# Optimization experiments

Measured on AMD Instinct MI355X. Metric: run time of the kernel, lower is better.

## Reference

```python
import jax, jax.numpy as jnp
import numpy as np

B, S, OBS, NINS, H, NBLK = 1024, 512, 5, 2, 32, 4
EPS = 1e-6


def setup_inputs() -> dict:
    key = jax.random.key(0)
    ks = jax.random.split(key, 10)
    obs_sequence = jax.random.normal(ks[0], (B, S, OBS), jnp.float32)
    prev_actions = jax.random.normal(ks[1], (B, S, NINS), jnp.float32)
    fan_in = OBS + NINS
    # xavier-uniform input projection
    lim_in = np.sqrt(6.0 / (fan_in + H))
    W_in = jax.random.uniform(ks[2], (H, fan_in), jnp.float32, -lim_in, lim_in)
    b_in = jnp.zeros((H,), jnp.float32)
    rms_w = jnp.ones((NBLK, H), jnp.float32)
    # LSTMCell default init: U(-1/sqrt(H), 1/sqrt(H)); gate order i,f,g,o
    s = 1.0 / np.sqrt(H)
    W_ih = jax.random.uniform(ks[3], (NBLK, 4 * H, H), jnp.float32, -s, s)
    W_hh = jax.random.uniform(ks[4], (NBLK, 4 * H, H), jnp.float32, -s, s)
    b_ih = jax.random.uniform(ks[5], (NBLK, 4 * H), jnp.float32, -s, s)
    b_hh = jax.random.uniform(ks[6], (NBLK, 4 * H), jnp.float32, -s, s)
    # heads: kaiming-uniform (linear, fan_in) scaled by 1e-3, zero bias
    lim_h = np.sqrt(3.0 / H)
    head_w = jax.random.uniform(ks[7], (NINS, H), jnp.float32, -lim_h, lim_h) * 1e-3
    head_b = jnp.zeros((NINS,), jnp.float32)
    return dict(obs_sequence=obs_sequence, prev_actions=prev_actions,
                W_in=W_in, b_in=b_in, rms_w=rms_w,
                W_ih=W_ih, W_hh=W_hh, b_ih=b_ih, b_hh=b_hh,
                head_w=head_w, head_b=head_b)


def reference(obs_sequence, prev_actions, W_in, b_in, rms_w,
              W_ih, W_hh, b_ih, b_hh, head_w, head_b):
    batch = obs_sequence.shape[0]
    hdim = W_in.shape[0]
    x = jnp.concatenate([obs_sequence, prev_actions], axis=-1) @ W_in.T + b_in  # [B,S,H]
    xs = jnp.swapaxes(x, 0, 1)  # [S,B,H] for scan over time
    h0 = jnp.zeros((NBLK, batch, hdim), x.dtype)
    c0 = jnp.zeros((NBLK, batch, hdim), x.dtype)

    def step(carry, xt):
        h, c = carry
        hs, cs = [], []
        for k in range(NBLK):  # small fixed stack of distinct blocks
            rms = jnp.sqrt(jnp.mean(xt * xt, axis=-1, keepdims=True) + EPS)
            xn = rms_w[k] * (xt / rms)
            gates = xn @ W_ih[k].T + b_ih[k] + h[k] @ W_hh[k].T + b_hh[k]  # [B,4H]
            i, f, g, o = jnp.split(gates, 4, axis=-1)
            c_new = jax.nn.sigmoid(f) * c[k] + jax.nn.sigmoid(i) * jnp.tanh(g)
            h_new = jax.nn.sigmoid(o) * jnp.tanh(c_new)
            xt = xt + h_new  # residual
            hs.append(h_new)
            cs.append(c_new)
        return (jnp.stack(hs), jnp.stack(cs)), xt

    (hT, cT), ys = jax.lax.scan(step, (h0, c0), xs)  # ys: [S,B,H]
    raw = jnp.einsum('sbh,ih->ibs', ys, head_w) + head_b[:, None, None]  # [NINS,B,S]
    out = jnp.sign(raw) * (jnp.exp(jnp.abs(raw)) - 1.0)  # symexp
    lim = jnp.array([5.0, 10.0], out.dtype)[:, None, None]
    out = jnp.clip(out, -lim, lim)
    return out, hT, cT
```

## Files before the change

### kernel.cpp

```cpp
#include <hip/hip_runtime.h>


constexpr int B_ = 1024, S_ = 512, OBS_ = 5, NINS_ = 2, H_ = 32, NBLK_ = 4;
constexpr int SUP_ = 4;
constexpr int TT_ = S_ / SUP_;
constexpr float EPS_ = 1e-6f;
constexpr float LOG2E_ = 1.4426950408889634f;

typedef __fp16 h2 __attribute__((ext_vector_type(2)));
typedef __fp16 h8 __attribute__((ext_vector_type(8)));
typedef float  f4 __attribute__((ext_vector_type(4)));
typedef int    i4 __attribute__((ext_vector_type(4)));

__device__ __forceinline__ float rcp_(float x) { return __builtin_amdgcn_rcpf(x); }
__device__ __forceinline__ float rsq_(float x) { return __builtin_amdgcn_rsqf(x); }
__device__ __forceinline__ float ex2_(float x) { return __builtin_amdgcn_exp2f(x); }
__device__ __forceinline__ h2 pk_(float a, float b) {
  return __builtin_amdgcn_cvt_pkrtz(a, b);
}
__device__ __forceinline__ h8 pk8_(f4 lo, f4 hi) {
  i4 q;
  q[0] = __builtin_bit_cast(int, pk_(lo[0], lo[1]));
  q[1] = __builtin_bit_cast(int, pk_(lo[2], lo[3]));
  q[2] = __builtin_bit_cast(int, pk_(hi[0], hi[1]));
  q[3] = __builtin_bit_cast(int, pk_(hi[2], hi[3]));
  return __builtin_bit_cast(h8, q);
}
__device__ __forceinline__ f4 mfma_(h8 a, h8 b, f4 c) {
  return __builtin_amdgcn_mfma_f32_16x16x32_f16(a, b, c, 0, 0, 0);
}
__device__ __forceinline__ f4 sg4_(f4 a) {
  f4 r;
  r[0] = rcp_(1.f + ex2_(-a[0]));
  r[1] = rcp_(1.f + ex2_(-a[1]));
  r[2] = rcp_(1.f + ex2_(-a[2]));
  r[3] = rcp_(1.f + ex2_(-a[3]));
  return r;
}
__device__ __forceinline__ f4 th4_(f4 a) {
  f4 r;
  r[0] = fmaf(2.f, rcp_(1.f + ex2_(-a[0])), -1.f);
  r[1] = fmaf(2.f, rcp_(1.f + ex2_(-a[1])), -1.f);
  r[2] = fmaf(2.f, rcp_(1.f + ex2_(-a[2])), -1.f);
  r[3] = fmaf(2.f, rcp_(1.f + ex2_(-a[3])), -1.f);
  return r;
}
__device__ __forceinline__ f4 thc4_(f4 c) {
  constexpr float M = 2.f * LOG2E_;
  f4 r;
  r[0] = fmaf(2.f, rcp_(1.f + ex2_(-M * c[0])), -1.f);
  r[1] = fmaf(2.f, rcp_(1.f + ex2_(-M * c[1])), -1.f);
  r[2] = fmaf(2.f, rcp_(1.f + ex2_(-M * c[2])), -1.f);
  r[3] = fmaf(2.f, rcp_(1.f + ex2_(-M * c[3])), -1.f);
  return r;
}
__device__ __forceinline__ float dot44_(f4 a, f4 x, f4 b2, f4 y) {
  float s = a[0] * x[0];
  s = fmaf(a[1], x[1], s); s = fmaf(a[2], x[2], s); s = fmaf(a[3], x[3], s);
  s = fmaf(b2[0], y[0], s); s = fmaf(b2[1], y[1], s);
  s = fmaf(b2[2], y[2], s); s = fmaf(b2[3], y[3], s);
  return s;
}
__device__ __forceinline__ float psw16_(float v, bool re) {
#if __has_builtin(__builtin_amdgcn_permlane16_swap)
  auto r = __builtin_amdgcn_permlane16_swap(
      __builtin_bit_cast(int, v), __builtin_bit_cast(int, v), false, false);
  return __builtin_bit_cast(float, re ? (int)r[1] : (int)r[0]);
#else
  return __shfl_xor(v, 16);
#endif
}
__device__ __forceinline__ float psw32_(float v, bool lo) {
#if __has_builtin(__builtin_amdgcn_permlane32_swap)
  auto r = __builtin_amdgcn_permlane32_swap(
      __builtin_bit_cast(int, v), __builtin_bit_cast(int, v), false, false);
  return __builtin_bit_cast(float, lo ? (int)r[1] : (int)r[0]);
#else
  return __shfl_xor(v, 32);
#endif
}

#define BLK_STEP(XT0, XT1) do {                                            \
    float _ss = dot44_((XT0), (XT1), (XT1), (XT0));                        \
    _ss = dot44_((XT0), (XT0), (XT1), (XT1));                              \
    _ss += psw16_(_ss, re_);                                               \
    _ss += psw32_(_ss, lo_);                                               \
    const float _rinv = rsq_(_ss * (1.0f / 32.0f) + EPS_);                 \
    const h8 _bh = pk8_(hv0, hv1);                                         \
    f4 _ah0 = mfma_(wh[0], _bh, biasv[0]);                                 \
    f4 _ah1 = mfma_(wh[1], _bh, biasv[1]);                                 \
    f4 _ah2 = mfma_(wh[2], _bh, biasv[2]);                                 \
    f4 _ah3 = mfma_(wh[3], _bh, biasv[3]);                                 \
    f4 _ah4 = mfma_(wh[4], _bh, biasv[4]);                                 \
    f4 _ah5 = mfma_(wh[5], _bh, biasv[5]);                                 \
    f4 _ah6 = mfma_(wh[6], _bh, biasv[6]);                                 \
    f4 _ah7 = mfma_(wh[7], _bh, biasv[7]);                                 \
    const f4 _rs0 = rw0v * _rinv, _rs1 = rw1v * _rinv;                     \
    const h8 _bx = pk8_((XT0) * _rs0, (XT1) * _rs1);                       \
    const f4 _gi0 = mfma_(wx[0], _bx, _ah0);                               \
    const f4 _gi1 = mfma_(wx[1], _bx, _ah1);                               \
    const f4 _gf0 = mfma_(wx[2], _bx, _ah2);                               \
    const f4 _gf1 = mfma_(wx[3], _bx, _ah3);                               \
    const f4 _gg0 = mfma_(wx[4], _bx, _ah4);                               \
    const f4 _gg1 = mfma_(wx[5], _bx, _ah5);                               \
    const f4 _go0 = mfma_(wx[6], _bx, _ah6);                               \
    const f4 _go1 = mfma_(wx[7], _bx, _ah7);                               \
    const f4 _si0 = sg4_(_gi0), _si1 = sg4_(_gi1);                         \
    const f4 _sf0 = sg4_(_gf0), _sf1 = sg4_(_gf1);                         \
    const f4 _tg0 = th4_(_gg0), _tg1 = th4_(_gg1);                         \
    const f4 _so0 = sg4_(_go0), _so1 = sg4_(_go1);                         \
    c0 = _sf0 * c0 + _si0 * _tg0;                                          \
    c1 = _sf1 * c1 + _si1 * _tg1;                                          \
    hv0 = _so0 * thc4_(c0);                                                \
    hv1 = _so1 * thc4_(c1);                                                \
    (XT0) += hv0;                                                          \
    (XT1) += hv1;                                                          \
  } while (0)

__global__ __launch_bounds__(256, 1) void garch_mfma6_kernel(
    const float* __restrict__ obs, const float* __restrict__ prev,
    const float* __restrict__ W_in, const float* __restrict__ b_in,
    const float* __restrict__ rms_w,
    const float* __restrict__ W_ih, const float* __restrict__ W_hh,
    const float* __restrict__ b_ih, const float* __restrict__ b_hh,
    const float* __restrict__ head_w, const float* __restrict__ head_b,
    float* __restrict__ out) {
  const int tid  = threadIdx.x;
  const int k    = tid >> 6;
  const int lane = tid & 63;
  const int g    = lane >> 4;
  const int b    = lane & 15;
  const int bg   = blockIdx.x * 16 + b;
  const bool re_ = ((lane >> 4) & 1) == 0;
  const bool lo_ = (lane < 32);

  __shared__ __align__(16) float xslot[3][2][SUP_][16][36];

  h8 wx[8], wh[8];
  f4 biasv[8];
  {
    const size_t wb = (size_t)k * 128 * 32;
#pragma unroll
    for (int mi = 0; mi < 8; ++mi) {
      const float scl = (mi == 4 || mi == 5) ? 2.f * LOG2E_ : LOG2E_;
      const int row = 16 * mi + b;
      const float* px = W_ih + wb + (size_t)row * 32;
      f4 x0 = *(const f4*)(px + 4 * g);
      f4 x1 = *(const f4*)(px + 16 + 4 * g);
      wx[mi] = pk8_(x0 * scl, x1 * scl);
      const float* ph = W_hh + wb + (size_t)row * 32;
      f4 h0v = *(const f4*)(ph + 4 * g);
      f4 h1v = *(const f4*)(ph + 16 + 4 * g);
      wh[mi] = pk8_(h0v * scl, h1v * scl);
      f4 bv;
#pragma unroll
      for (int r = 0; r < 4; ++r) {
        const int gr = k * 128 + 16 * mi + 4 * g + r;
        bv[r] = (b_ih[gr] + b_hh[gr]) * scl;
      }
      biasv[mi] = bv;
    }
  }
  f4 rw0v, rw1v;
#pragma unroll
  for (int r = 0; r < 4; ++r) {
    rw0v[r] = rms_w[k * 32 + 4 * g + r];
    rw1v[r] = rms_w[k * 32 + 16 + 4 * g + r];
  }

  h8 winA0 = {}, winA1 = {};
  f4 bin0v = {}, bin1v = {};
  const float* obs_b = nullptr; const float* prev_b = nullptr;
  f4 cin[SUP_] = {}, nin[SUP_] = {};
  if (k == 0) {
    f4 lo0, lo1; const f4 z = {};
#pragma unroll
    for (int r = 0; r < 4; ++r) {
      const int kk = 4 * g + r;
      lo0[r] = (kk < 7) ? W_in[(size_t)b * 7 + kk] : 0.f;
      lo1[r] = (kk < 7) ? W_in[(size_t)(16 + b) * 7 + kk] : 0.f;
    }
    winA0 = pk8_(lo0, z);
    winA1 = pk8_(lo1, z);
#pragma unroll
    for (int r = 0; r < 4; ++r) {
      bin0v[r] = b_in[4 * g + r];
      bin1v[r] = b_in[16 + 4 * g + r];
    }
    obs_b  = obs  + (size_t)bg * S_ * OBS_;
    prev_b = prev + (size_t)bg * S_ * NINS_;
#pragma unroll
    for (int s = 0; s < SUP_; ++s) {
      const float* o = obs_b + (size_t)s * OBS_;
      if (g == 0)      { cin[s][0] = o[0]; cin[s][1] = o[1]; cin[s][2] = o[2]; cin[s][3] = o[3]; }
      else if (g == 1) { cin[s][0] = o[4]; cin[s][1] = prev_b[2 * s]; cin[s][2] = prev_b[2 * s + 1]; cin[s][3] = 0.f; }
    }
  }
  f4 hw00 = {}, hw01 = {}, hw10 = {}, hw11 = {};
  float hb0 = 0.f, hb1 = 0.f;
  if (k == 3) {
#pragma unroll
    for (int r = 0; r < 4; ++r) {
      hw00[r] = head_w[4 * g + r]      * LOG2E_;
      hw01[r] = head_w[16 + 4 * g + r] * LOG2E_;
      hw10[r] = head_w[32 + 4 * g + r] * LOG2E_;
      hw11[r] = head_w[48 + 4 * g + r] * LOG2E_;
    }
    hb0 = head_b[0] * LOG2E_;
    hb1 = head_b[1] * LOG2E_;
  }

  f4 c0 = {}, c1 = {}, hv0 = {}, hv1 = {};

  float* out_y  = out;
  float* out_hT = out + (size_t)NINS_ * B_ * S_;
  float* out_cT = out_hT + (size_t)NBLK_ * B_ * H_;

  for (int tau = 0; tau < TT_ + NBLK_ - 1; ++tau) {
    __syncthreads();
    const int tt = tau - k;
    if (tt < 0 || tt >= TT_) continue;
    const int t0 = SUP_ * tt;
    const int wp = tau & 1, rp = (tau + 1) & 1;

    f4 x0[SUP_], x1[SUP_];
    if (k == 0) {
      if (tt + 1 < TT_) {
#pragma unroll
        for (int s = 0; s < SUP_; ++s) {
          const int t = t0 + SUP_ + s;
          const float* o = obs_b + (size_t)t * OBS_;
          if (g == 0)      { nin[s][0] = o[0]; nin[s][1] = o[1]; nin[s][2] = o[2]; nin[s][3] = o[3]; }
          else if (g == 1) { nin[s][0] = o[4]; nin[s][1] = prev_b[2 * t]; nin[s][2] = prev_b[2 * t + 1]; nin[s][3] = 0.f; }
        }
      }
      const f4 z = {};
#pragma unroll
      for (int s = 0; s < SUP_; ++s) {
        const h8 binp = pk8_(cin[s], z);
        x0[s] = mfma_(winA0, binp, bin0v);
        x1[s] = mfma_(winA1, binp, bin1v);
      }
    } else {
#pragma unroll
      for (int s = 0; s < SUP_; ++s) {
        x0[s] = *(const f4*)&xslot[k - 1][rp][s][b][4 * g];
        x1[s] = *(const f4*)&xslot[k - 1][rp][s][b][16 + 4 * g];
      }
    }

#pragma unroll
    for (int s = 0; s < SUP_; ++s) {
      BLK_STEP(x0[s], x1[s]);
    }

    if (k < 3) {
#pragma unroll
      for (int s = 0; s < SUP_; ++s) {
        *(f4*)&xslot[k][wp][s][b][4 * g]      = x0[s];
        *(f4*)&xslot[k][wp][s][b][16 + 4 * g] = x1[s];
      }
    } else {
      float p0[SUP_], p1[SUP_];
#pragma unroll
      for (int s = 0; s < SUP_; ++s) {
        float a = dot44_(hw00, x0[s], hw01, x1[s]);
        float bq = dot44_(hw10, x0[s], hw11, x1[s]);
        a += psw16_(a, re_); a += psw32_(a, lo_);
        bq += psw16_(bq, re_); bq += psw32_(bq, lo_);
        p0[s] = a + hb0;
        p1[s] = bq + hb1;
      }
      if (lane < 16) {
        f4 v0, v1;
#pragma unroll
        for (int s = 0; s < SUP_; ++s) {
          v0[s] = copysignf(fminf(ex2_(fabsf(p0[s])) - 1.f, 5.f),  p0[s]);
          v1[s] = copysignf(fminf(ex2_(fabsf(p1[s])) - 1.f, 10.f), p1[s]);
        }
        *(f4*)&out_y[(size_t)bg * S_ + t0]                   = v0;
        *(f4*)&out_y[(size_t)B_ * S_ + (size_t)bg * S_ + t0] = v1;
      }
    }

    if (tt == TT_ - 1) {
      float* hp = out_hT + ((size_t)k * B_ + bg) * H_;
      float* cp = out_cT + ((size_t)k * B_ + bg) * H_;
#pragma unroll
      for (int r = 0; r < 4; ++r) {
        hp[4 * g + r]      = hv0[r];
        hp[16 + 4 * g + r] = hv1[r];
        cp[4 * g + r]      = c0[r];
        cp[16 + 4 * g + r] = c1[r];
      }
    }

    if (k == 0) {
#pragma unroll
      for (int s = 0; s < SUP_; ++s) cin[s] = nin[s];
    }
  }
}

extern "C" void kernel_launch(void* const* d_in, const int* in_sizes, int n_in,
                              void* d_out, int out_size, void* d_ws, size_t ws_size,
                              hipStream_t stream) {
  (void)in_sizes; (void)n_in; (void)d_ws; (void)ws_size; (void)out_size;
  garch_mfma6_kernel<<<dim3(B_ / 16), dim3(256), 0, stream>>>(
      (const float*)d_in[0],
      (const float*)d_in[1],
      (const float*)d_in[2],
      (const float*)d_in[3],
      (const float*)d_in[4],
      (const float*)d_in[5],
      (const float*)d_in[6],
      (const float*)d_in[7],
      (const float*)d_in[8],
      (const float*)d_in[9],
      (const float*)d_in[10],
      (float*)d_out);
}
```

Before: 465.8 us.

## Hoist input-gate MFMAs off recurrence chain and merge activation reciprocals

Splits each block step so the RMS-norm and input-projection MFMAs for all SUP_ sub-steps are issued together before the recurrent loop, leaving only the hidden-state MFMAs on the serial dependency chain. The gate activations are rewritten to share reciprocals: sigmoid(i)*tanh(g) and sigmoid(o)*tanh(c) are each computed with one rcp over a product of denominators, cutting transcendental ops. This costs more live registers for the precomputed gate tiles (32 f4 values) and risks overflow or inf in the combined denominators for large gate magnitudes.

```diff
diff --git a/kernel.cpp b/kernel.cpp
--- a/kernel.cpp
+++ b/kernel.cpp
@@ -29,29 +29,16 @@
 __device__ __forceinline__ f4 mfma_(h8 a, h8 b, f4 c) {
   return __builtin_amdgcn_mfma_f32_16x16x32_f16(a, b, c, 0, 0, 0);
 }
-__device__ __forceinline__ f4 sg4_(f4 a) {
+__device__ __forceinline__ f4 e4n_(f4 a) {
   f4 r;
-  r[0] = rcp_(1.f + ex2_(-a[0]));
-  r[1] = rcp_(1.f + ex2_(-a[1]));
-  r[2] = rcp_(1.f + ex2_(-a[2]));
-  r[3] = rcp_(1.f + ex2_(-a[3]));
+  r[0] = ex2_(-a[0]); r[1] = ex2_(-a[1]);
+  r[2] = ex2_(-a[2]); r[3] = ex2_(-a[3]);
   return r;
 }
-__device__ __forceinline__ f4 th4_(f4 a) {
+__device__ __forceinline__ f4 rcp4_(f4 a) {
   f4 r;
-  r[0] = fmaf(2.f, rcp_(1.f + ex2_(-a[0])), -1.f);
-  r[1] = fmaf(2.f, rcp_(1.f + ex2_(-a[1])), -1.f);
-  r[2] = fmaf(2.f, rcp_(1.f + ex2_(-a[2])), -1.f);
-  r[3] = fmaf(2.f, rcp_(1.f + ex2_(-a[3])), -1.f);
-  return r;
-}
-__device__ __forceinline__ f4 thc4_(f4 c) {
-  constexpr float M = 2.f * LOG2E_;
-  f4 r;
-  r[0] = fmaf(2.f, rcp_(1.f + ex2_(-M * c[0])), -1.f);
-  r[1] = fmaf(2.f, rcp_(1.f + ex2_(-M * c[1])), -1.f);
-  r[2] = fmaf(2.f, rcp_(1.f + ex2_(-M * c[2])), -1.f);
-  r[3] = fmaf(2.f, rcp_(1.f + ex2_(-M * c[3])), -1.f);
+  r[0] = rcp_(a[0]); r[1] = rcp_(a[1]);
+  r[2] = rcp_(a[2]); r[3] = rcp_(a[3]);
   return r;
 }
 __device__ __forceinline__ float dot44_(f4 a, f4 x, f4 b2, f4 y) {
@@ -80,44 +67,20 @@
 #endif
 }
 
-#define BLK_STEP(XT0, XT1) do {                                            \
-    float _ss = dot44_((XT0), (XT1), (XT1), (XT0));                        \
-    _ss = dot44_((XT0), (XT0), (XT1), (XT1));                              \
-    _ss += psw16_(_ss, re_);                                               \
-    _ss += psw32_(_ss, lo_);                                               \
-    const float _rinv = rsq_(_ss * (1.0f / 32.0f) + EPS_);                 \
-    const h8 _bh = pk8_(hv0, hv1);                                         \
-    f4 _ah0 = mfma_(wh[0], _bh, biasv[0]);                                 \
-    f4 _ah1 = mfma_(wh[1], _bh, biasv[1]);                                 \
-    f4 _ah2 = mfma_(wh[2], _bh, biasv[2]);                                 \
-    f4 _ah3 = mfma_(wh[3], _bh, biasv[3]);                                 \
-    f4 _ah4 = mfma_(wh[4], _bh, biasv[4]);                                 \
-    f4 _ah5 = mfma_(wh[5], _bh, biasv[5]);                                 \
-    f4 _ah6 = mfma_(wh[6], _bh, biasv[6]);                                 \
-    f4 _ah7 = mfma_(wh[7], _bh, biasv[7]);                                 \
-    const f4 _rs0 = rw0v * _rinv, _rs1 = rw1v * _rinv;                     \
-    const h8 _bx = pk8_((XT0) * _rs0, (XT1) * _rs1);                       \
-    const f4 _gi0 = mfma_(wx[0], _bx, _ah0);                               \
-    const f4 _gi1 = mfma_(wx[1], _bx, _ah1);                               \
-    const f4 _gf0 = mfma_(wx[2], _bx, _ah2);                               \
-    const f4 _gf1 = mfma_(wx[3], _bx, _ah3);                               \
-    const f4 _gg0 = mfma_(wx[4], _bx, _ah4);                               \
-    const f4 _gg1 = mfma_(wx[5], _bx, _ah5);                               \
-    const f4 _go0 = mfma_(wx[6], _bx, _ah6);                               \
-    const f4 _go1 = mfma_(wx[7], _bx, _ah7);                               \
-    const f4 _si0 = sg4_(_gi0), _si1 = sg4_(_gi1);                         \
-    const f4 _sf0 = sg4_(_gf0), _sf1 = sg4_(_gf1);                         \
-    const f4 _tg0 = th4_(_gg0), _tg1 = th4_(_gg1);                         \
-    const f4 _so0 = sg4_(_go0), _so1 = sg4_(_go1);                         \
-    c0 = _sf0 * c0 + _si0 * _tg0;                                          \
-    c1 = _sf1 * c1 + _si1 * _tg1;                                          \
-    hv0 = _so0 * thc4_(c0);                                                \
-    hv1 = _so1 * thc4_(c1);                                                \
-    (XT0) += hv0;                                                          \
-    (XT1) += hv1;                                                          \
+#define ACT_TILE(GI, GF, GG, GO, C, HV) do {                               \
+    const f4 _one = {1.f, 1.f, 1.f, 1.f};                                  \
+    const f4 _Ei = e4n_(GI);                                               \
+    const f4 _Eg = e4n_(GG);                                               \
+    const f4 _Ef = e4n_(GF);                                               \
+    const f4 _sitg = (_one - _Eg) * rcp4_((_one + _Ei) * (_one + _Eg));    \
+    const f4 _sf = rcp4_(_one + _Ef);                                      \
+    (C) = _sf * (C) + _sitg;                                               \
+    const f4 _Eo = e4n_(GO);                                               \
+    const f4 _Ec = e4n_((C) * (2.f * LOG2E_));                             \
+    (HV) = (_one - _Ec) * rcp4_((_one + _Eo) * (_one + _Ec));              \
   } while (0)
 
-__global__ __launch_bounds__(256, 1) void garch_mfma6_kernel(
+__global__ __launch_bounds__(256, 1) void garch_mfma7_kernel(
     const float* __restrict__ obs, const float* __restrict__ prev,
     const float* __restrict__ W_in, const float* __restrict__ b_in,
     const float* __restrict__ rms_w,
@@ -249,9 +212,39 @@
       }
     }
 
+    h8 bx[SUP_];
 #pragma unroll
     for (int s = 0; s < SUP_; ++s) {
-      BLK_STEP(x0[s], x1[s]);
+      float ss = dot44_(x0[s], x0[s], x1[s], x1[s]);
+      ss += psw16_(ss, re_);
+      ss += psw32_(ss, lo_);
+      const float rinv = rsq_(ss * (1.0f / 32.0f) + EPS_);
+      bx[s] = pk8_(x0[s] * (rw0v * rinv), x1[s] * (rw1v * rinv));
+    }
+    f4 gx[SUP_][8];
+#pragma unroll
+    for (int s = 0; s < SUP_; ++s) {
+#pragma unroll
+      for (int m = 0; m < 8; ++m) {
+        gx[s][m] = mfma_(wx[m], bx[s], biasv[m]);
+      }
+    }
+
+#pragma unroll
+    for (int s = 0; s < SUP_; ++s) {
+      const h8 bh = pk8_(hv0, hv1);
+      const f4 gi0 = mfma_(wh[0], bh, gx[s][0]);
+      const f4 gi1 = mfma_(wh[1], bh, gx[s][1]);
+      const f4 gf0 = mfma_(wh[2], bh, gx[s][2]);
+      const f4 gf1 = mfma_(wh[3], bh, gx[s][3]);
+      const f4 gg0 = mfma_(wh[4], bh, gx[s][4]);
+      const f4 gg1 = mfma_(wh[5], bh, gx[s][5]);
+      const f4 go0 = mfma_(wh[6], bh, gx[s][6]);
+      const f4 go1 = mfma_(wh[7], bh, gx[s][7]);
+      ACT_TILE(gi0, gf0, gg0, go0, c0, hv0);
+      ACT_TILE(gi1, gf1, gg1, go1, c1, hv1);
+      x0[s] += hv0;
+      x1[s] += hv1;
     }
 
     if (k < 3) {
@@ -306,7 +299,7 @@
                               void* d_out, int out_size, void* d_ws, size_t ws_size,
                               hipStream_t stream) {
   (void)in_sizes; (void)n_in; (void)d_ws; (void)ws_size; (void)out_size;
-  garch_mfma6_kernel<<<dim3(B_ / 16), dim3(256), 0, stream>>>(
+  garch_mfma7_kernel<<<dim3(B_ / 16), dim3(256), 0, stream>>>(
       (const float*)d_in[0],
       (const float*)d_in[1],
       (const float*)d_in[2],
```

New measurement: 429.4 us. -7.8%, faster.
